# Optimization experiments

Hardware: AMD Instinct MI355X
Metric: run time of the kernel (lower is better)

Reference implementation:

```python
import jax, jax.numpy as jnp
import numpy as np

DIM = 1024
NUM_HEADS = 16
HEAD_D = DIM // NUM_HEADS


def setup_inputs() -> dict:
    key = jax.random.key(0)
    ks = jax.random.split(key, 9)
    B, T, D = 4, 2048, DIM
    s = 1.0 / np.sqrt(D)
    return {
        "x": jax.random.normal(ks[0], (B, T, D), dtype=jnp.float32),
        "Wq": jax.random.normal(ks[1], (D, D), dtype=jnp.float32) * s,
        "bq": jnp.zeros((D,), dtype=jnp.float32),
        "Wk": jax.random.normal(ks[2], (D, D), dtype=jnp.float32) * s,
        "bk": jnp.zeros((D,), dtype=jnp.float32),
        "Wv": jax.random.normal(ks[3], (D, D), dtype=jnp.float32) * s,
        "bv": jnp.zeros((D,), dtype=jnp.float32),
        "Wo": jax.random.normal(ks[4], (D, D), dtype=jnp.float32) * s,
        "bo": jnp.zeros((D,), dtype=jnp.float32),
    }


def reference(x, Wq, bq, Wk, bk, Wv, bv, Wo, bo):
    B, T, D = x.shape
    H, Hd = NUM_HEADS, HEAD_D
    # QKV projections (torch Linear: x @ W.T + b)
    q = (x @ Wq.T + bq).reshape(B, T, H, Hd).transpose(0, 2, 1, 3)  # [B,H,T,Hd]
    k = (x @ Wk.T + bk).reshape(B, T, H, Hd).transpose(0, 2, 1, 3)
    v = (x @ Wv.T + bv).reshape(B, T, H, Hd).transpose(0, 2, 1, 3)
    scores = jnp.einsum("bhqd,bhkd->bhqk", q, k) / jnp.sqrt(jnp.float32(Hd))
    probs = jax.nn.softmax(scores, axis=-1)
    out = jnp.einsum("bhqk,bhkd->bhqd", probs, v)  # [B,H,T,Hd]
    out = out.transpose(0, 2, 1, 3).reshape(B, T, D)
    return out @ Wo.T + bo
```

## Files before the change

kernel.cpp:

```cpp
#include <hip/hip_runtime.h>

typedef unsigned short u16;
typedef unsigned int   u32;
typedef __bf16 bf16;
typedef __attribute__((ext_vector_type(8))) __bf16 bf16x8;
typedef __attribute__((ext_vector_type(4))) float  f32x4;


__device__ __forceinline__ u16 f2bf(float f) {
  u32 u = __float_as_uint(f);
  u32 r = (u + 0x7fffu + ((u >> 16) & 1u)) >> 16;
  return (u16)r;
}

__device__ __forceinline__ void gload_lds16(const void* g, void* l) {
  __builtin_amdgcn_global_load_lds((__attribute__((address_space(1))) u32*)g,
                                   (__attribute__((address_space(3))) u32*)l,
                                   16, 0, 0);
}

__device__ __forceinline__ u32 cvt_pk_bf16(float lo, float hi) {
  u32 r;
  asm("v_cvt_pk_bf16_f32 %0, %1, %2" : "=v"(r) : "v"(lo), "v"(hi));
  return r;
}

#define SCL_LOG2E 0.1803368801111204f


__global__ __launch_bounds__(256) void cvt_bf16_kernel(const float* __restrict__ in,
                                                       u16* __restrict__ out, int n4) {
  int i = blockIdx.x * blockDim.x + threadIdx.x;
  int stride = gridDim.x * blockDim.x;
  for (; i < n4; i += stride) {
    float4 v = ((const float4*)in)[i];
    uint2 o;
    o.x = (u32)f2bf(v.x) | ((u32)f2bf(v.y) << 16);
    o.y = (u32)f2bf(v.z) | ((u32)f2bf(v.w) << 16);
    ((uint2*)out)[i] = o;
  }
}

__global__ __launch_bounds__(256) void cvt4_kernel(const float* __restrict__ p0,
                                                   const float* __restrict__ p1,
                                                   const float* __restrict__ p2,
                                                   const float* __restrict__ p3,
                                                   u16* o0, u16* o1, u16* o2, u16* o3) {
  const int which = blockIdx.x >> 8;
  const float* in = which == 0 ? p0 : which == 1 ? p1 : which == 2 ? p2 : p3;
  u16* out = which == 0 ? o0 : which == 1 ? o1 : which == 2 ? o2 : o3;
  int i = (blockIdx.x & 255) * 256 + threadIdx.x;
  #pragma unroll
  for (int r = 0; r < 4; ++r, i += 65536) {
    float4 v = ((const float4*)in)[i];
    uint2 o;
    o.x = (u32)f2bf(v.x) | ((u32)f2bf(v.y) << 16);
    o.y = (u32)f2bf(v.z) | ((u32)f2bf(v.w) << 16);
    ((uint2*)out)[i] = o;
  }
}


#define GK 1024
#define GN 1024

__global__ __launch_bounds__(256) void gemm_qkv_kernel(const u16* __restrict__ A,
                                                       const u16* __restrict__ Wq,
                                                       const u16* __restrict__ Wk,
                                                       const u16* __restrict__ Wv,
                                                       const float* __restrict__ bq,
                                                       const float* __restrict__ bk,
                                                       const float* __restrict__ bv,
                                                       u16* __restrict__ Qo,
                                                       u16* __restrict__ Ko,
                                                       u16* __restrict__ Vo) {
  __shared__ u16 sA[2][128 * 32];
  __shared__ u16 sB[2][128 * 32];

  const int tid  = threadIdx.x;
  const int lane = tid & 63;
  const int w    = tid >> 6;
  const int wm   = w >> 1, wn = w & 1;
  const int lid  = (blockIdx.x & 7) * 192 + (blockIdx.x >> 3);
  const int which = lid >> 9;
  const int sub   = lid & 511;
  const u16*  W    = which == 0 ? Wq : which == 1 ? Wk : Wv;
  const float* bias = which == 0 ? bq : which == 1 ? bk : bv;
  const int tn   = sub & 7;
  const int tm   = sub >> 3;
  const int m0   = tm * 128, n0 = tn * 128;
  const int rgrp = lane >> 4, rlo = lane & 15;

  const int c0 = (w * 2 + 0) * 64 + lane;
  const int c1 = (w * 2 + 1) * 64 + lane;
  const int r0 = c0 >> 2, col0 = (((c0 & 3) ^ (r0 & 3)) * 8);
  const int r1 = c1 >> 2, col1 = (((c1 & 3) ^ (r1 & 3)) * 8);
  const u16* aS0 = A + (size_t)(m0 + r0) * GK + col0;
  const u16* aS1 = A + (size_t)(m0 + r1) * GK + col1;
  const u16* bS0 = W + (size_t)(n0 + r0) * GK + col0;
  const u16* bS1 = W + (size_t)(n0 + r1) * GK + col1;

  auto stage = [&](u16* dA, u16* dB, int kt) {
    int k0 = kt * 32;
    gload_lds16(aS0 + k0, dA + (w * 2 + 0) * 512);
    gload_lds16(aS1 + k0, dA + (w * 2 + 1) * 512);
    gload_lds16(bS0 + k0, dB + (w * 2 + 0) * 512);
    gload_lds16(bS1 + k0, dB + (w * 2 + 1) * 512);
  };

  f32x4 acc[4][4] = {};

  auto compute = [&](const u16* sAc, const u16* sBc) {
    bf16x8 a[4], b[4];
    #pragma unroll
    for (int i = 0; i < 4; ++i) {
      int row = wm * 64 + i * 16 + rlo;
      int cb  = rgrp ^ (row & 3);
      a[i] = *(const bf16x8*)&sAc[row * 32 + cb * 8];
    }
    #pragma unroll
    for (int j = 0; j < 4; ++j) {
      int row = wn * 64 + j * 16 + rlo;
      int cb  = rgrp ^ (row & 3);
      b[j] = *(const bf16x8*)&sBc[row * 32 + cb * 8];
    }
    #pragma unroll
    for (int i = 0; i < 4; ++i)
      #pragma unroll
      for (int j = 0; j < 4; ++j)
        acc[i][j] = __builtin_amdgcn_mfma_f32_16x16x32_bf16(a[i], b[j], acc[i][j], 0, 0, 0);
  };

  stage(sA[0], sB[0], 0);
  asm volatile("s_waitcnt vmcnt(0)" ::: "memory");
  __syncthreads();

  for (int kt = 0; kt < GK / 32; kt += 2) {
    stage(sA[1], sB[1], kt + 1);
    compute(sA[0], sB[0]);
    asm volatile("s_waitcnt vmcnt(0)" ::: "memory");
    __syncthreads();
    if (kt + 2 < GK / 32) stage(sA[0], sB[0], kt + 2);
    compute(sA[1], sB[1]);
    asm volatile("s_waitcnt vmcnt(0)" ::: "memory");
    __syncthreads();
  }

  if (which <= 1) {
    u16* out = which == 0 ? Qo : Ko;
    const float scl = which == 0 ? 1.0f : SCL_LOG2E;
    #pragma unroll
    for (int i = 0; i < 4; ++i)
      #pragma unroll
      for (int j = 0; j < 4; ++j)
        #pragma unroll
        for (int r = 0; r < 4; ++r) {
          int m = m0 + wm * 64 + i * 16 + rgrp * 4 + r;
          int n = n0 + wn * 64 + j * 16 + rlo;
          float v = (acc[i][j][r] + bias[n]) * scl;
          out[(size_t)m * GN + n] = (u16)__builtin_bit_cast(u16, (bf16)v);
        }
  } else {
    #pragma unroll
    for (int i = 0; i < 4; ++i)
      #pragma unroll
      for (int j = 0; j < 4; ++j) {
        int mb = m0 + wm * 64 + i * 16 + rgrp * 4;
        int n  = n0 + wn * 64 + j * 16 + rlo;
        int b = mb >> 11, t = mb & 2047, h = n >> 6, hd = n & 63;
        float bv_ = bias[n];
        uint2 st;
        st.x = cvt_pk_bf16(acc[i][j][0] + bv_, acc[i][j][1] + bv_);
        st.y = cvt_pk_bf16(acc[i][j][2] + bv_, acc[i][j][3] + bv_);
        *(uint2*)&Vo[((size_t)(b * 16 + h) * 64 + hd) * 2048 + t] = st;
      }
  }
}

__global__ __launch_bounds__(256) void gemm_out_kernel(const u16* __restrict__ A,
                                                       const u16* __restrict__ W,
                                                       const float* __restrict__ bias,
                                                       float* __restrict__ Cout) {
  __shared__ u16 sA[2][128 * 32];
  __shared__ u16 sB[2][128 * 32];

  const int tid  = threadIdx.x;
  const int lane = tid & 63;
  const int w    = tid >> 6;
  const int wm   = w >> 1, wn = w & 1;
  const int lid  = (blockIdx.x & 7) * 64 + (blockIdx.x >> 3);
  const int tn   = lid & 7;
  const int tm   = lid >> 3;
  const int m0   = tm * 128, n0 = tn * 128;
  const int rgrp = lane >> 4, rlo = lane & 15;

  const int c0 = (w * 2 + 0) * 64 + lane;
  const int c1 = (w * 2 + 1) * 64 + lane;
  const int r0 = c0 >> 2, col0 = (((c0 & 3) ^ (r0 & 3)) * 8);
  const int r1 = c1 >> 2, col1 = (((c1 & 3) ^ (r1 & 3)) * 8);
  const u16* aS0 = A + (size_t)(m0 + r0) * GK + col0;
  const u16* aS1 = A + (size_t)(m0 + r1) * GK + col1;
  const u16* bS0 = W + (size_t)(n0 + r0) * GK + col0;
  const u16* bS1 = W + (size_t)(n0 + r1) * GK + col1;

  auto stage = [&](u16* dA, u16* dB, int kt) {
    int k0 = kt * 32;
    gload_lds16(aS0 + k0, dA + (w * 2 + 0) * 512);
    gload_lds16(aS1 + k0, dA + (w * 2 + 1) * 512);
    gload_lds16(bS0 + k0, dB + (w * 2 + 0) * 512);
    gload_lds16(bS1 + k0, dB + (w * 2 + 1) * 512);
  };

  f32x4 acc[4][4] = {};

  auto compute = [&](const u16* sAc, const u16* sBc) {
    bf16x8 a[4], b[4];
    #pragma unroll
    for (int i = 0; i < 4; ++i) {
      int row = wm * 64 + i * 16 + rlo;
      int cb  = rgrp ^ (row & 3);
      a[i] = *(const bf16x8*)&sAc[row * 32 + cb * 8];
    }
    #pragma unroll
    for (int j = 0; j < 4; ++j) {
      int row = wn * 64 + j * 16 + rlo;
      int cb  = rgrp ^ (row & 3);
      b[j] = *(const bf16x8*)&sBc[row * 32 + cb * 8];
    }
    #pragma unroll
    for (int i = 0; i < 4; ++i)
      #pragma unroll
      for (int j = 0; j < 4; ++j)
        acc[i][j] = __builtin_amdgcn_mfma_f32_16x16x32_bf16(a[i], b[j], acc[i][j], 0, 0, 0);
  };

  stage(sA[0], sB[0], 0);
  asm volatile("s_waitcnt vmcnt(0)" ::: "memory");
  __syncthreads();

  for (int kt = 0; kt < GK / 32; kt += 2) {
    stage(sA[1], sB[1], kt + 1);
    compute(sA[0], sB[0]);
    asm volatile("s_waitcnt vmcnt(0)" ::: "memory");
    __syncthreads();
    if (kt + 2 < GK / 32) stage(sA[0], sB[0], kt + 2);
    compute(sA[1], sB[1]);
    asm volatile("s_waitcnt vmcnt(0)" ::: "memory");
    __syncthreads();
  }

  #pragma unroll
  for (int i = 0; i < 4; ++i)
    #pragma unroll
    for (int j = 0; j < 4; ++j)
      #pragma unroll
      for (int r = 0; r < 4; ++r) {
        int m = m0 + wm * 64 + i * 16 + rgrp * 4 + r;
        int n = n0 + wn * 64 + j * 16 + rlo;
        Cout[(size_t)m * GN + n] = acc[i][j][r] + bias[n];
      }
}


__global__ __launch_bounds__(256) void attn_kernel(const u16* __restrict__ Q,
                                                   const u16* __restrict__ K,
                                                   const u16* __restrict__ Vt,
                                                   bf16* __restrict__ O) {
  __shared__ u16 sK[2][64 * 64];
  __shared__ u16 sV[2][64 * 64];

  const int tid  = threadIdx.x;
  const int lane = tid & 63;
  const int w    = tid >> 6;
  const int rgrp = lane >> 4, rlo = lane & 15;
  const int bid  = (blockIdx.x & 7) * 128 + (blockIdx.x >> 3);
  const int qt   = bid & 15;
  const int bh   = bid >> 4;
  const int b    = bh >> 4, h = bh & 15;

  const u16* Qh = Q  + (size_t)b * 2048 * 1024 + h * 64;
  const u16* Kh = K  + (size_t)b * 2048 * 1024 + h * 64;
  const u16* Vh = Vt + (size_t)bh * 64 * 2048;

  const int c0 = (w * 2 + 0) * 64 + lane;
  const int c1 = (w * 2 + 1) * 64 + lane;
  const int r0 = c0 >> 3, col0 = ((c0 & 7) ^ (r0 & 7)) * 8;
  const int r1 = c1 >> 3, col1 = ((c1 & 7) ^ (r1 & 7)) * 8;
  const u16* kb0 = Kh + (size_t)r0 * 1024 + col0;
  const u16* kb1 = Kh + (size_t)r1 * 1024 + col1;
  const u16* vb0 = Vh + (size_t)r0 * 2048 + col0;
  const u16* vb1 = Vh + (size_t)r1 * 2048 + col1;

  auto stage = [&](u16* dK, u16* dV) {
    gload_lds16(kb0, dK + (w * 2 + 0) * 512);
    gload_lds16(kb1, dK + (w * 2 + 1) * 512);
    gload_lds16(vb0, dV + (w * 2 + 0) * 512);
    gload_lds16(vb1, dV + (w * 2 + 1) * 512);
    kb0 += 65536; kb1 += 65536;
    vb0 += 64;    vb1 += 64;
  };

  stage(sK[0], sV[0]);

  bf16x8 bQ[2][2];
  #pragma unroll
  for (int qg = 0; qg < 2; ++qg) {
    int q0 = qt * 128 + w * 32 + qg * 16 + rlo;
    bQ[qg][0] = *(const bf16x8*)&Qh[(size_t)q0 * 1024 + rgrp * 8];
    bQ[qg][1] = *(const bf16x8*)&Qh[(size_t)q0 * 1024 + 32 + rgrp * 8];
  }

  bf16x8 vones;
  #pragma unroll
  for (int i = 0; i < 8; ++i) vones[i] = (bf16)1.0f;
  const f32x4 FZ = {0.f, 0.f, 0.f, 0.f};

  asm volatile("s_waitcnt vmcnt(0)" ::: "memory");
  __syncthreads();

  f32x4 lden[2] = {};
  f32x4 o[2][4] = {};

  auto iter = [&](const u16* sKc, const u16* sVc, u16* sKn, u16* sVn, int t) {
    if (t + 1 < 32) stage(sKn, sVn);

    f32x4 sT[2][4];
    __builtin_amdgcn_s_setprio(1);
    #pragma unroll
    for (int nt = 0; nt < 4; ++nt) {
      int row = nt * 16 + rlo;
      int cb0_ = (0 + rgrp) ^ (row & 7);
      int cb1_ = (4 + rgrp) ^ (row & 7);
      bf16x8 aK0 = *(const bf16x8*)&sKc[row * 64 + cb0_ * 8];
      bf16x8 aK1 = *(const bf16x8*)&sKc[row * 64 + cb1_ * 8];
      sT[0][nt] = __builtin_amdgcn_mfma_f32_16x16x32_bf16(aK0, bQ[0][0], FZ, 0, 0, 0);
      sT[1][nt] = __builtin_amdgcn_mfma_f32_16x16x32_bf16(aK0, bQ[1][0], FZ, 0, 0, 0);
      sT[0][nt] = __builtin_amdgcn_mfma_f32_16x16x32_bf16(aK1, bQ[0][1], sT[0][nt], 0, 0, 0);
      sT[1][nt] = __builtin_amdgcn_mfma_f32_16x16x32_bf16(aK1, bQ[1][1], sT[1][nt], 0, 0, 0);
    }
    __builtin_amdgcn_s_setprio(0);

    #pragma unroll
    for (int qg = 0; qg < 2; ++qg) {
      #pragma unroll
      for (int nt = 0; nt < 4; ++nt)
        #pragma unroll
        for (int r = 0; r < 4; ++r)
          sT[qg][nt][r] = __builtin_amdgcn_exp2f(sT[qg][nt][r]);

      u32 pw[4][2];
      #pragma unroll
      for (int nt = 0; nt < 4; ++nt) {
        pw[nt][0] = cvt_pk_bf16(sT[qg][nt][0], sT[qg][nt][1]);
        pw[nt][1] = cvt_pk_bf16(sT[qg][nt][2], sT[qg][nt][3]);
      }
      bf16x8 bP[2];
      #pragma unroll
      for (int kk = 0; kk < 2; ++kk) {
        u32 a0 = pw[2 * kk][0], b0 = pw[2 * kk + 1][0];
        u32 a1 = pw[2 * kk][1], b1 = pw[2 * kk + 1][1];
        asm("v_permlane32_swap_b32 %0, %1" : "+v"(a0), "+v"(b0));
        asm("v_permlane16_swap_b32 %0, %1" : "+v"(a0), "+v"(b0));
        asm("v_permlane32_swap_b32 %0, %1" : "+v"(a1), "+v"(b1));
        asm("v_permlane16_swap_b32 %0, %1" : "+v"(a1), "+v"(b1));
        union { u32 u[4]; bf16x8 v; } fu;
        fu.u[0] = a0; fu.u[1] = a1; fu.u[2] = b0; fu.u[3] = b1;
        bP[kk] = fu.v;
      }

      __builtin_amdgcn_s_setprio(1);
      #pragma unroll
      for (int kk = 0; kk < 2; ++kk) {
        lden[qg] = __builtin_amdgcn_mfma_f32_16x16x32_bf16(vones, bP[kk], lden[qg], 0, 0, 0);
        #pragma unroll
        for (int dt = 0; dt < 4; ++dt) {
          int rowv = dt * 16 + rlo;
          int cbv  = (kk * 4 + rgrp) ^ (rowv & 7);
          bf16x8 aV = *(const bf16x8*)&sVc[rowv * 64 + cbv * 8];
          o[qg][dt] = __builtin_amdgcn_mfma_f32_16x16x32_bf16(aV, bP[kk], o[qg][dt], 0, 0, 0);
        }
      }
      __builtin_amdgcn_s_setprio(0);
    }

    asm volatile("s_waitcnt vmcnt(0)" ::: "memory");
    __syncthreads();
  };

  for (int t = 0; t < 32; t += 2) {
    iter(sK[0], sV[0], sK[1], sV[1], t);
    iter(sK[1], sV[1], sK[0], sV[0], t + 1);
  }

  #pragma unroll
  for (int qg = 0; qg < 2; ++qg) {
    const float inv = 1.0f / lden[qg][0];
    const int tq = qt * 128 + w * 32 + qg * 16 + rlo;
    #pragma unroll
    for (int dt = 0; dt < 4; ++dt) {
      uint2 st;
      st.x = cvt_pk_bf16(o[qg][dt][0] * inv, o[qg][dt][1] * inv);
      st.y = cvt_pk_bf16(o[qg][dt][2] * inv, o[qg][dt][3] * inv);
      *(uint2*)&O[((size_t)(b * 2048 + tq)) * 1024 + h * 64 + dt * 16 + rgrp * 4] = st;
    }
  }
}


extern "C" void kernel_launch(void* const* d_in, const int* in_sizes, int n_in,
                              void* d_out, int out_size, void* d_ws, size_t ws_size,
                              hipStream_t stream) {
  const float* x  = (const float*)d_in[0];
  const float* Wq = (const float*)d_in[1];
  const float* bq = (const float*)d_in[2];
  const float* Wk = (const float*)d_in[3];
  const float* bk = (const float*)d_in[4];
  const float* Wv = (const float*)d_in[5];
  const float* bv = (const float*)d_in[6];
  const float* Wo = (const float*)d_in[7];
  const float* bo = (const float*)d_in[8];

  char* ws = (char*)d_ws;
  u16* xb  = (u16*)(ws);
  u16* Wqb = (u16*)(ws + 16777216);
  u16* Wkb = (u16*)(ws + 18874368);
  u16* Wvb = (u16*)(ws + 20971520);
  u16* Wob = (u16*)(ws + 23068672);
  u16* Qb  = (u16*)(ws + 25165824);
  u16* Kb  = (u16*)(ws + 41943040);
  u16* Vtb = (u16*)(ws + 58720256);
  u16* Ab  = (u16*)(ws + 75497472);

  cvt_bf16_kernel<<<4096, 256, 0, stream>>>(x, xb, 8388608 / 4);
  cvt4_kernel<<<1024, 256, 0, stream>>>(Wq, Wk, Wv, Wo, Wqb, Wkb, Wvb, Wob);

  gemm_qkv_kernel<<<1536, 256, 0, stream>>>(xb, Wqb, Wkb, Wvb, bq, bk, bv, Qb, Kb, Vtb);

  attn_kernel<<<1024, 256, 0, stream>>>(Qb, Kb, Vtb, (bf16*)Ab);

  gemm_out_kernel<<<512, 256, 0, stream>>>(Ab, Wob, bo, (float*)d_out);
}
```

Baseline: 211.8 us.

## Use partial vmcnt waits to split attention K/V pipeline and drop GEMM waits

The attention loop is split into a QK phase and a softmax/PV phase. After QK it waits only on the K loads (partial vmcnt) so the V tile can still be in flight while scores are computed, with explicit s_barrier plus sched_barrier between phases. The last tile is peeled out of the loop. In both projection GEMMs the explicit vmcnt(0) waits before __syncthreads are removed, relying on the compiler to order the async global-to-LDS loads. That relies on the compiler's implicit waits being sufficient, which risks an LDS race if they are not. The attention path also now runs two barriers per iteration instead of one.

```diff
diff --git a/kernel.cpp b/kernel.cpp
--- a/kernel.cpp
+++ b/kernel.cpp
@@ -132,17 +132,14 @@
   };
 
   stage(sA[0], sB[0], 0);
-  asm volatile("s_waitcnt vmcnt(0)" ::: "memory");
   __syncthreads();
 
   for (int kt = 0; kt < GK / 32; kt += 2) {
     stage(sA[1], sB[1], kt + 1);
     compute(sA[0], sB[0]);
-    asm volatile("s_waitcnt vmcnt(0)" ::: "memory");
     __syncthreads();
     if (kt + 2 < GK / 32) stage(sA[0], sB[0], kt + 2);
     compute(sA[1], sB[1]);
-    asm volatile("s_waitcnt vmcnt(0)" ::: "memory");
     __syncthreads();
   }
 
@@ -235,17 +232,14 @@
   };
 
   stage(sA[0], sB[0], 0);
-  asm volatile("s_waitcnt vmcnt(0)" ::: "memory");
   __syncthreads();
 
   for (int kt = 0; kt < GK / 32; kt += 2) {
     stage(sA[1], sB[1], kt + 1);
     compute(sA[0], sB[0]);
-    asm volatile("s_waitcnt vmcnt(0)" ::: "memory");
     __syncthreads();
     if (kt + 2 < GK / 32) stage(sA[0], sB[0], kt + 2);
     compute(sA[1], sB[1]);
-    asm volatile("s_waitcnt vmcnt(0)" ::: "memory");
     __syncthreads();
   }
 
@@ -316,15 +310,14 @@
   const f32x4 FZ = {0.f, 0.f, 0.f, 0.f};
 
   asm volatile("s_waitcnt vmcnt(0)" ::: "memory");
-  __syncthreads();
+  __builtin_amdgcn_s_barrier();
+  __builtin_amdgcn_sched_barrier(0);
 
   f32x4 lden[2] = {};
   f32x4 o[2][4] = {};
-
-  auto iter = [&](const u16* sKc, const u16* sVc, u16* sKn, u16* sVn, int t) {
-    if (t + 1 < 32) stage(sKn, sVn);
-
-    f32x4 sT[2][4];
+  f32x4 sT[2][4];
+
+  auto qk = [&](const u16* sKc) {
     __builtin_amdgcn_s_setprio(1);
     #pragma unroll
     for (int nt = 0; nt < 4; ++nt) {
@@ -339,7 +332,9 @@
       sT[1][nt] = __builtin_amdgcn_mfma_f32_16x16x32_bf16(aK1, bQ[1][1], sT[1][nt], 0, 0, 0);
     }
     __builtin_amdgcn_s_setprio(0);
-
+  };
+
+  auto smpv = [&](const u16* sVc) {
     #pragma unroll
     for (int qg = 0; qg < 2; ++qg) {
       #pragma unroll
@@ -382,15 +377,31 @@
       }
       __builtin_amdgcn_s_setprio(0);
     }
-
-    asm volatile("s_waitcnt vmcnt(0)" ::: "memory");
-    __syncthreads();
-  };
-
-  for (int t = 0; t < 32; t += 2) {
-    iter(sK[0], sV[0], sK[1], sV[1], t);
-    iter(sK[1], sV[1], sK[0], sV[0], t + 1);
-  }
+  };
+
+  auto iter = [&](const u16* sKc, const u16* sVc, u16* sKn, u16* sVn) {
+    stage(sKn, sVn);
+    qk(sKc);
+    asm volatile("s_waitcnt vmcnt(4)" ::: "memory");
+    __builtin_amdgcn_s_barrier();
+    __builtin_amdgcn_sched_barrier(0);
+    smpv(sVc);
+    asm volatile("s_waitcnt vmcnt(2)" ::: "memory");
+    __builtin_amdgcn_s_barrier();
+    __builtin_amdgcn_sched_barrier(0);
+  };
+
+  for (int it = 0; it < 15; ++it) {
+    iter(sK[0], sV[0], sK[1], sV[1]);
+    iter(sK[1], sV[1], sK[0], sV[0]);
+  }
+  iter(sK[0], sV[0], sK[1], sV[1]);
+
+  qk(sK[1]);
+  asm volatile("s_waitcnt vmcnt(0)" ::: "memory");
+  __builtin_amdgcn_s_barrier();
+  __builtin_amdgcn_sched_barrier(0);
+  smpv(sV[1]);
 
   #pragma unroll
   for (int qg = 0; qg < 2; ++qg) {
```

Measured after the change: 213.3 us. About the same (+0.7%).
